# Performance work log

Measured on AMD Instinct MI355X. Metric: run time of the kernel, lower is better.

## Reference

```python
import jax, jax.numpy as jnp
import numpy as np

R = 4        # downsample / window size
HEADS = 8
TOPK = 4


def _dwconv3x3(x_nchw, w, b):
    # depthwise 3x3, padding 1. w: [C,1,3,3]
    C = x_nchw.shape[1]
    y = jax.lax.conv_general_dilated(
        x_nchw, w, window_strides=(1, 1), padding=((1, 1), (1, 1)),
        dimension_numbers=('NCHW', 'OIHW', 'NCHW'), feature_group_count=C)
    return y + b[None, :, None, None]


def setup_inputs() -> dict:
    key = jax.random.key(0)
    ks = jax.random.split(key, 8)
    B, H, W, C = 8, 64, 64, 384
    s = 0.02
    return {
        'x': jax.random.normal(ks[0], (B, H, W, C), jnp.float32),
        'qkv_w': jax.random.normal(ks[1], (3 * C, C), jnp.float32) * s,
        'dwx_w': jax.random.normal(ks[2], (C, 1, 3, 3), jnp.float32) * s,
        'dwx_b': jax.random.normal(ks[3], (C,), jnp.float32) * s,
        'dw_w': jax.random.normal(ks[4], (C, 1, 3, 3), jnp.float32) * s,
        'dw_b': jax.random.normal(ks[5], (C,), jnp.float32) * s,
        'pw_w': jax.random.normal(ks[6], (C, C), jnp.float32) * s,
        'pw_b': jax.random.normal(ks[7], (C,), jnp.float32) * s,
    }


def reference(x, qkv_w, dwx_w, dwx_b, dw_w, dw_b, pw_w, pw_b):
    B, H, W, C = x.shape
    h, r, topk = HEADS, R, TOPK
    d = C // h
    scale = d ** -0.5
    Hc, Wc = H // r, W // r
    Nc = Hc * Wc

    y = x

    # ---- coarse stream: avg-pool downsample then dense attention ----
    xc = x.reshape(B, Hc, r, Wc, r, C).mean(axis=(2, 4))       # [B,Hc,Wc,C]
    xc = xc.reshape(B, Nc, C)
    qkv = (xc @ qkv_w.T).reshape(B, Nc, 3, h, d).transpose(2, 0, 3, 1, 4)
    q, k, v = qkv[0], qkv[1], qkv[2]                           # [B,h,Nc,d]
    attn = jnp.einsum('bhqd,bhkd->bhqk', q, k) * scale         # [B,h,Nc,Nc]
    _, indices = jax.lax.top_k(attn, topk)                     # [B,h,Nc,topk]
    attn = jax.nn.softmax(attn, axis=-1)
    xo = jnp.einsum('bhqk,bhkd->bhqd', attn, v)                # [B,h,Nc,d]
    xo = xo.transpose(0, 2, 1, 3).reshape(B, Hc, Wc, C)

    # ---- full-res stream: windowed sparse attention driven by topk indices ----
    yf = y.reshape(B, H * W, C)
    QKV = (yf @ qkv_w.T).reshape(B, H * W, 3, h, d).transpose(2, 0, 3, 1, 4)
    Q, K, V = QKV[0], QKV[1], QKV[2]                           # [B,h,H*W,d]

    def to_windows(t):
        # [B,h,H*W,d] -> [B,h,nWin,r*r,d], window order matches coarse (h w) flatten
        t = t.reshape(B, h, Hc, r, Wc, r, d).transpose(0, 1, 2, 4, 3, 5, 6)
        return t.reshape(B, h, Nc, r * r, d)

    Qw, Kw, Vw = to_windows(Q), to_windows(K), to_windows(V)

    idx = indices[:, :, :, :, None, None]                      # [B,h,Nc,topk,1,1]
    Kg = jnp.take_along_axis(Kw[:, :, None], idx, axis=3)      # [B,h,Nc,topk,r*r,d]
    Vg = jnp.take_along_axis(Vw[:, :, None], idx, axis=3)
    Kg = Kg.reshape(B, h, Nc, topk * r * r, d)
    Vg = Vg.reshape(B, h, Nc, topk * r * r, d)

    a2 = jnp.einsum('bhnqd,bhnkd->bhnqk', Qw, Kg) * scale
    a2 = jax.nn.softmax(a2, axis=-1)
    yo = jnp.einsum('bhnqk,bhnkd->bhnqd', a2, Vg)              # [B,h,Nc,r*r,d]
    yo = yo.reshape(B, h, Hc, Wc, r, r, d).transpose(0, 2, 4, 3, 5, 1, 6)
    yo = yo.reshape(B, H, W, C)                                # NHWC

    # ---- coarse branch: nearest upsample + depthwise conv ----
    xn = xo.transpose(0, 3, 1, 2)                              # [B,C,Hc,Wc]
    xn = jnp.repeat(jnp.repeat(xn, r, axis=2), r, axis=3)      # [B,C,H,W]
    xn = _dwconv3x3(xn, dwx_w, dwx_b)
    xn = xn.transpose(0, 2, 3, 1)                              # NHWC

    # ---- fuse, depthwise + pointwise conv ----
    z = 0.5 * xn + 0.5 * yo
    z = z.transpose(0, 3, 1, 2)                                # NCHW
    z = _dwconv3x3(z, dw_w, dw_b)
    z = jnp.einsum('bchw,oc->bohw', z, pw_w) + pw_b[None, :, None, None]
    return z.transpose(0, 2, 3, 1)                             # NHWC
```

## Files before the change

kernel.cpp:

```cpp
#include <hip/hip_runtime.h>
#include <hip/hip_bf16.h>


#define Bq 8
#define Hh 8
#define Dd 48
#define Cc 384
#define NC 256
#define MFINE 32768
#define KDIM 384
#define SCALE 0.14433756729740643f

typedef __attribute__((ext_vector_type(8))) short short8;
typedef __attribute__((ext_vector_type(4))) short short4v;
typedef __attribute__((ext_vector_type(4))) float floatx4;

#define QKVW_PLANE 12582912

#define WS_XBF   88342528
#define WS_XC     9437184
#define WS_WQKV 113508352
#define WS_WDWX 114393088
#define WS_BDWX 114400000
#define WS_WDW  114400768
#define WS_BDW  114407680
#define WS_WPW  114408448
#define WS_BPW  114703360

__global__ __launch_bounds__(256) void k_detect(const ushort* x, int* flag) {
    __shared__ int cnt;
    if (threadIdx.x == 0) cnt = 0;
    __syncthreads();
    int c = 0;
    for (int i = threadIdx.x; i < 8192; i += 256) {
        int e = (x[i] >> 7) & 0xFF;
        if (e >= 0xC1) c++;
    }
    atomicAdd(&cnt, c);
    __syncthreads();
    if (threadIdx.x == 0) *flag = (cnt > 16) ? 1 : 0;
}

__device__ __forceinline__ void cvt_seg(const void* src, __hip_bfloat16* dst, int blk, int n4, int fl) {
    int i = blk * 256 + threadIdx.x;
    if (i >= n4) return;
    if (fl) {
        floatx4 v = ((const floatx4*)src)[i];
        short4v o;
        for (int t = 0; t < 4; t++) {
            __hip_bfloat16 hb = __float2bfloat16(v[t]);
            o[t] = *(short*)&hb;
        }
        ((short4v*)dst)[i] = o;
    } else {
        ((short4v*)dst)[i] = ((const short4v*)src)[i];
    }
}

__global__ __launch_bounds__(256) void k_cvt_pool(
        const void* sx, const void* s1, const void* s2, const void* s3,
        const void* s4, const void* s5, const void* s6, const void* s7,
        char* ws, const int* flag) {
    int blk = blockIdx.x;
    int fl = *flag;
    if (blk < 12288) { cvt_seg(sx, (__hip_bfloat16*)(ws + WS_XBF),  blk,          3145728, fl); return; }
    if (blk < 12720) { cvt_seg(s1, (__hip_bfloat16*)(ws + WS_WQKV), blk - 12288,  110592, fl); return; }
    if (blk < 12724) { cvt_seg(s2, (__hip_bfloat16*)(ws + WS_WDWX), blk - 12720,  864,    fl); return; }
    if (blk < 12725) { cvt_seg(s3, (__hip_bfloat16*)(ws + WS_BDWX), blk - 12724,  96,     fl); return; }
    if (blk < 12729) { cvt_seg(s4, (__hip_bfloat16*)(ws + WS_WDW),  blk - 12725,  864,    fl); return; }
    if (blk < 12730) { cvt_seg(s5, (__hip_bfloat16*)(ws + WS_BDW),  blk - 12729,  96,     fl); return; }
    if (blk < 12874) { cvt_seg(s6, (__hip_bfloat16*)(ws + WS_WPW),  blk - 12730,  36864,  fl); return; }
    if (blk < 12875) { cvt_seg(s7, (__hip_bfloat16*)(ws + WS_BPW),  blk - 12874,  96,     fl); return; }
    int pb = blk - 12875;
    if (threadIdx.x >= 192) return;
    int b = pb >> 8, n = pb & 255;
    int yc = n >> 4, xcc = n & 15;
    int c0 = threadIdx.x * 2;
    size_t pixbase = (((size_t)(b * 64 + yc * 4)) * 64 + xcc * 4) * Cc + c0;
    float s0 = 0.f, s1v = 0.f;
    if (fl) {
        const float* xf = (const float*)sx;
        for (int i = 0; i < 4; i++)
            for (int j = 0; j < 4; j++) {
                float2 u = *(const float2*)(xf + pixbase + ((size_t)i * 64 + j) * Cc);
                s0 += u.x; s1v += u.y;
            }
    } else {
        const ushort* xb = (const ushort*)sx;
        for (int i = 0; i < 4; i++)
            for (int j = 0; j < 4; j++) {
                uint u = *(const uint*)(xb + pixbase + ((size_t)i * 64 + j) * Cc);
                s0 += __uint_as_float(u << 16);
                s1v += __uint_as_float(u & 0xFFFF0000u);
            }
    }
    __hip_bfloat16 h0 = __float2bfloat16(s0 * 0.0625f), h1 = __float2bfloat16(s1v * 0.0625f);
    uint uo = (uint)*(ushort*)&h0 | ((uint)*(ushort*)&h1 << 16);
    *(uint*)((ushort*)(ws + WS_XC) + (size_t)pb * Cc + c0) = uo;
}

__device__ __forceinline__ void gload_lds16(const ushort* g, short* l) {
    __builtin_amdgcn_global_load_lds(
        (const __attribute__((address_space(1))) unsigned int*)(g),
        (__attribute__((address_space(3))) unsigned int*)(l), 16, 0, 0);
}

__device__ __forceinline__ void gemm128_dbuf(const ushort* A, const ushort* B,
                                             int tile_m, int tile_n,
                                             short* As, short* Bs, floatx4 (&acc)[4][4]) {
    int lane = threadIdx.x & 63, wave = threadIdx.x >> 6;
    int m_off = (wave >> 1) * 64, n_off = (wave & 1) * 64;
    int row16 = lane & 15, quad = lane >> 4;
    int srow = lane >> 3;
    int scol = (((lane & 7) ^ srow) * 8);
    for (int i = 0; i < 4; i++)
        for (int j = 0; j < 4; j++)
            acc[i][j] = (floatx4){0.f, 0.f, 0.f, 0.f};
    int rsw = (row16 & 7) * 8;
#define STG(buf, k0)                                                                          \
    for (int g = wave; g < 16; g += 4) {                                                      \
        gload_lds16(A + (size_t)(tile_m + g * 8 + srow) * KDIM + (k0) + scol, As + (buf) * 8192 + g * 512); \
        gload_lds16(B + (size_t)(tile_n + g * 8 + srow) * KDIM + (k0) + scol, Bs + (buf) * 8192 + g * 512); \
    }
    STG(0, 0)
    int cur = 0;
    for (int k0 = 0; k0 < KDIM; k0 += 64) {
        if (k0 + 64 < KDIM) {
            STG(cur ^ 1, k0 + 64)
            asm volatile("s_waitcnt vmcnt(8)" ::: "memory");
        } else {
            asm volatile("s_waitcnt vmcnt(0)" ::: "memory");
        }
        __builtin_amdgcn_s_barrier();
        __builtin_amdgcn_sched_barrier(0);
        __builtin_amdgcn_s_setprio(1);
        const short* Ab = As + cur * 8192;
        const short* Bb = Bs + cur * 8192;
        for (int h = 0; h < 2; h++) {
            short8 af[4], bf[4];
            for (int mt = 0; mt < 4; mt++)
                af[mt] = *(const short8*)(Ab + (m_off + mt * 16 + row16) * 64 + (((h * 4 + quad) * 8) ^ rsw));
            for (int nt = 0; nt < 4; nt++)
                bf[nt] = *(const short8*)(Bb + (n_off + nt * 16 + row16) * 64 + (((h * 4 + quad) * 8) ^ rsw));
            for (int mt = 0; mt < 4; mt++)
                for (int nt = 0; nt < 4; nt++)
                    acc[mt][nt] = __builtin_amdgcn_mfma_f32_16x16x32_bf16(af[mt], bf[nt], acc[mt][nt], 0, 0, 0);
        }
        __builtin_amdgcn_s_setprio(0);
        __builtin_amdgcn_sched_barrier(0);
        __builtin_amdgcn_s_barrier();
        cur ^= 1;
    }
#undef STG
}

__device__ __forceinline__ void gemm128_sb(const ushort* A, const ushort* B,
                                           int tile_m, int tile_n,
                                           short* As, short* Bs, floatx4 (&acc)[4][4]) {
    int lane = threadIdx.x & 63, wave = threadIdx.x >> 6;
    int m_off = (wave >> 1) * 64, n_off = (wave & 1) * 64;
    int row16 = lane & 15, quad = lane >> 4;
    int srow = lane >> 3;
    int scol = (((lane & 7) ^ srow) * 8);
    for (int i = 0; i < 4; i++)
        for (int j = 0; j < 4; j++)
            acc[i][j] = (floatx4){0.f, 0.f, 0.f, 0.f};
    int rsw = (row16 & 7) * 8;
    for (int k0 = 0; k0 < KDIM; k0 += 64) {
        for (int g = wave; g < 16; g += 4) {
            gload_lds16(A + (size_t)(tile_m + g * 8 + srow) * KDIM + k0 + scol, As + g * 512);
            gload_lds16(B + (size_t)(tile_n + g * 8 + srow) * KDIM + k0 + scol, Bs + g * 512);
        }
        __syncthreads();
        for (int h = 0; h < 2; h++) {
            short8 af[4], bf[4];
            for (int mt = 0; mt < 4; mt++)
                af[mt] = *(const short8*)(As + (m_off + mt * 16 + row16) * 64 + (((h * 4 + quad) * 8) ^ rsw));
            for (int nt = 0; nt < 4; nt++)
                bf[nt] = *(const short8*)(Bs + (n_off + nt * 16 + row16) * 64 + (((h * 4 + quad) * 8) ^ rsw));
            for (int mt = 0; mt < 4; mt++)
                for (int nt = 0; nt < 4; nt++)
                    acc[mt][nt] = __builtin_amdgcn_mfma_f32_16x16x32_bf16(af[mt], bf[nt], acc[mt][nt], 0, 0, 0);
        }
        __syncthreads();
    }
}

__device__ __forceinline__ floatx4 mfma_tile(const ushort* A, const ushort* W,
                                             int tile_m, int tile_n, int lane) {
    int row16 = lane & 15, quad = lane >> 4;
    const ushort* arow = A + (size_t)(tile_m + row16) * KDIM + quad * 8;
    const ushort* brow = W + (size_t)(tile_n + row16) * KDIM + quad * 8;
    floatx4 acc = {0.f, 0.f, 0.f, 0.f};
    for (int kk = 0; kk < KDIM; kk += 32) {
        short8 af = *(const short8*)(arow + kk);
        short8 bf = *(const short8*)(brow + kk);
        acc = __builtin_amdgcn_mfma_f32_16x16x32_bf16(af, bf, acc, 0, 0, 0);
    }
    return acc;
}

__global__ __launch_bounds__(256) void k_gemm_qkv_coarse(const ushort* A, const ushort* W,
                                                         __hip_bfloat16* qh, __hip_bfloat16* ql,
                                                         __hip_bfloat16* kh, __hip_bfloat16* kl,
                                                         __hip_bfloat16* vt) {
    int lane = threadIdx.x & 63, wave = threadIdx.x >> 6;
    int tile_m = blockIdx.y * 32 + (wave >> 1) * 16;
    int tile_n = blockIdx.x * 32 + (wave & 1) * 16;
    floatx4 acc = mfma_tile(A, W, tile_m, tile_n, lane);
    int row16 = lane & 15, quad = lane >> 4;
    int n = tile_n + row16;
    int which = n / Cc, hd = n % Cc, head = hd / Dd, dim = hd % Dd;
    for (int rr = 0; rr < 4; rr++) {
        int m = tile_m + quad * 4 + rr;
        int b = m >> 8, nc = m & 255;
        float v = acc[rr];
        __hip_bfloat16 hi = __float2bfloat16(v);
        if (which == 0) {
            size_t p = ((size_t)((b * Hh + head) * NC + nc)) * Dd + dim;
            qh[p] = hi;
            ql[p] = __float2bfloat16(v - __bfloat162float(hi));
        } else if (which == 1) {
            size_t p = ((size_t)((b * Hh + head) * NC + nc)) * Dd + dim;
            kh[p] = hi;
            kl[p] = __float2bfloat16(v - __bfloat162float(hi));
        } else {
            vt[((size_t)((b * Hh + head) * Dd + dim)) * NC + nc] = hi;
        }
    }
}

#define PST 264
__global__ __launch_bounds__(256) void k_fine_cattn(
        const ushort* A, const ushort* W, __hip_bfloat16* qkvw,
        const ushort* qh, const ushort* ql, const ushort* kh, const ushort* kl,
        const ushort* vt, int* idx_out, __hip_bfloat16* xo) {
    __shared__ __align__(16) short smem[32768];
    int lane = threadIdx.x & 63, wave = threadIdx.x >> 6;
    int row16 = lane & 15, quad = lane >> 4;
    if (blockIdx.x < 256) {
        short* Pl = smem;
        int bh = blockIdx.x >> 2, qt = blockIdx.x & 3;
        int q0 = qt * 64 + wave * 16;
        short8 zf = {0, 0, 0, 0, 0, 0, 0, 0};
        const ushort* qhr = qh + ((size_t)(bh * NC + q0 + row16)) * Dd;
        const ushort* qlr = ql + ((size_t)(bh * NC + q0 + row16)) * Dd;
        short8 aqh0 = *(const short8*)(qhr + quad * 8);
        short8 aqh1 = (quad < 2) ? *(const short8*)(qhr + 32 + quad * 8) : zf;
        short8 aql0 = *(const short8*)(qlr + quad * 8);
        short8 aql1 = (quad < 2) ? *(const short8*)(qlr + 32 + quad * 8) : zf;
        floatx4 s[16];
        for (int nt = 0; nt < 16; nt++) {
            const ushort* khr = kh + ((size_t)(bh * NC + nt * 16 + row16)) * Dd;
            const ushort* klr = kl + ((size_t)(bh * NC + nt * 16 + row16)) * Dd;
            short8 bh0 = *(const short8*)(khr + quad * 8);
            short8 bh1 = (quad < 2) ? *(const short8*)(khr + 32 + quad * 8) : zf;
            short8 bl0 = *(const short8*)(klr + quad * 8);
            short8 bl1 = (quad < 2) ? *(const short8*)(klr + 32 + quad * 8) : zf;
            floatx4 a = {0.f, 0.f, 0.f, 0.f};
            a = __builtin_amdgcn_mfma_f32_16x16x32_bf16(aqh0, bh0, a, 0, 0, 0);
            a = __builtin_amdgcn_mfma_f32_16x16x32_bf16(aqh1, bh1, a, 0, 0, 0);
            a = __builtin_amdgcn_mfma_f32_16x16x32_bf16(aqh0, bl0, a, 0, 0, 0);
            a = __builtin_amdgcn_mfma_f32_16x16x32_bf16(aqh1, bl1, a, 0, 0, 0);
            a = __builtin_amdgcn_mfma_f32_16x16x32_bf16(aql0, bh0, a, 0, 0, 0);
            a = __builtin_amdgcn_mfma_f32_16x16x32_bf16(aql1, bh1, a, 0, 0, 0);
            s[nt] = a;
        }
        for (int rr = 0; rr < 4; rr++) {
            float sv[16];
            for (int nt = 0; nt < 16; nt++) sv[nt] = s[nt][rr] * SCALE;
            int chosen[4] = {-1, -1, -1, -1};
            float rowmax = 0.f;
            for (int it = 0; it < 4; it++) {
                float bv = -3.402823e38f; int bi = 0x7fffffff;
                for (int nt = 0; nt < 16; nt++) {
                    int ki = nt * 16 + row16;
                    bool skip = (ki == chosen[0]) | (ki == chosen[1]) | (ki == chosen[2]) | (ki == chosen[3]);
                    if (!skip && sv[nt] > bv) { bv = sv[nt]; bi = ki; }
                }
                for (int mk = 1; mk < 16; mk <<= 1) {
                    float ov = __shfl_xor(bv, mk); int oi = __shfl_xor(bi, mk);
                    if (ov > bv || (ov == bv && oi < bi)) { bv = ov; bi = oi; }
                }
                chosen[it] = bi;
                if (it == 0) rowmax = bv;
            }
            if (row16 == 0) {
                int q = q0 + quad * 4 + rr;
                for (int it = 0; it < 4; it++)
                    idx_out[((size_t)bh * NC + q) * 4 + it] = chosen[it];
            }
            float ex[16], sum = 0.f;
            for (int nt = 0; nt < 16; nt++) { ex[nt] = __expf(sv[nt] - rowmax); sum += ex[nt]; }
            for (int mk = 1; mk < 16; mk <<= 1) sum += __shfl_xor(sum, mk);
            float inv = 1.f / sum;
            for (int nt = 0; nt < 16; nt++) {
                __hip_bfloat16 hb = __float2bfloat16(ex[nt] * inv);
                Pl[(wave * 16 + quad * 4 + rr) * PST + nt * 16 + row16] = *(short*)&hb;
            }
        }
        const ushort* vbase = vt + (size_t)bh * Dd * NC;
        floatx4 o[3];
        for (int i = 0; i < 3; i++) o[i] = (floatx4){0.f, 0.f, 0.f, 0.f};
        for (int k0 = 0; k0 < 256; k0 += 32) {
            short8 pa = *(const short8*)&Pl[(wave * 16 + row16) * PST + k0 + quad * 8];
            for (int d2 = 0; d2 < 3; d2++) {
                short8 vb = *(const short8*)(vbase + (size_t)(d2 * 16 + row16) * NC + k0 + quad * 8);
                o[d2] = __builtin_amdgcn_mfma_f32_16x16x32_bf16(pa, vb, o[d2], 0, 0, 0);
            }
        }
        int b = bh >> 3, hh = bh & 7;
        for (int rr = 0; rr < 4; rr++) {
            int q = q0 + quad * 4 + rr;
            size_t base = ((size_t)(b * NC + q)) * Cc + hh * Dd;
            for (int d2 = 0; d2 < 3; d2++)
                xo[base + d2 * 16 + row16] = __float2bfloat16(o[d2][rr]);
        }
        return;
    }
    floatx4 acc[4][4];
    int f = blockIdx.x - 256;
    int s = (f & 7) * 288 + (f >> 3);
    int by = s / 9, bx = s - by * 9;
    int tile_m = by * 128, tile_n = bx * 128;
    gemm128_dbuf(A, W, tile_m, tile_n, smem, smem + 16384, acc);
    int m_off = (wave >> 1) * 64, n_off = (wave & 1) * 64;
    short* epi = smem + wave * 2304;
    int r = lane >> 1, parity = lane & 1;
    for (int half = 0; half < 2; half++) {
        __syncthreads();
        for (int mt2 = 0; mt2 < 2; mt2++) {
            int mt = half * 2 + mt2;
            for (int nt = 0; nt < 4; nt++)
                for (int rr = 0; rr < 4; rr++) {
                    __hip_bfloat16 hb = __float2bfloat16(acc[mt][nt][rr]);
                    epi[(mt2 * 16 + quad * 4 + rr) * 72 + nt * 16 + row16] = *(short*)&hb;
                }
        }
        __syncthreads();
        int m = tile_m + m_off + half * 32 + r;
        int b = m >> 12, pix = m & 4095;
        int y = pix >> 6, x = pix & 63;
        int win = (y >> 2) * 16 + (x >> 2);
        int pos = (y & 3) * 4 + (x & 3);
        size_t mrow = ((size_t)b * Hh * NC * 16 * Dd) + ((size_t)win * 16 + pos) * Dd;
        for (int i = 0; i < 4; i++) {
            int j = parity + 2 * i;
            int n = tile_n + n_off + j * 8;
            int which = n / Cc, hd = n % Cc, head = hd / Dd, dim = hd % Dd;
            short8 val = *(const short8*)(epi + r * 72 + j * 8);
            size_t dst = (size_t)which * QKVW_PLANE + (size_t)head * (NC * 16 * Dd) + mrow + dim;
            *(short8*)((ushort*)qkvw + dst) = val;
        }
    }
}

#define PSTRIDE 80
#define VSTRIDE 72
__global__ __launch_bounds__(256) void k_win_attn(const __hip_bfloat16* qkvw, const int* idx, __hip_bfloat16* yo) {
    __shared__ __align__(16) short Pl[4][16 * PSTRIDE];
    __shared__ __align__(16) short Vt[4][48 * VSTRIDE];
    int lane = threadIdx.x & 63, wave = threadIdx.x >> 6;
    int gw = blockIdx.x * 4 + wave;
    int bh = gw >> 8, n = gw & 255;
    int row16 = lane & 15, quad = lane >> 4;
    const ushort* qb  = (const ushort*)qkvw + (size_t)(bh * NC + n) * 768;
    const ushort* kwb = (const ushort*)qkvw + (size_t)QKVW_PLANE + (size_t)bh * NC * 768;
    const ushort* vwb = (const ushort*)qkvw + 2 * (size_t)QKVW_PLANE + (size_t)bh * NC * 768;
    int sel[4];
    for (int g = 0; g < 4; g++) sel[g] = idx[(size_t)gw * 4 + g];
    const ushort* vrow = vwb + (size_t)sel[quad] * 768 + row16 * 48;
    short8 vv[6];
    for (int i = 0; i < 6; i++) vv[i] = *(const short8*)(vrow + i * 8);
    short8 zf = {0, 0, 0, 0, 0, 0, 0, 0};
    short8 aq0 = *(const short8*)(qb + row16 * 48 + quad * 8);
    short8 aq1 = (quad < 2) ? *(const short8*)(qb + row16 * 48 + 32 + quad * 8) : zf;
    floatx4 s[4];
    for (int nt = 0; nt < 4; nt++) {
        const ushort* kb = kwb + (size_t)sel[nt] * 768 + row16 * 48;
        short8 bk0 = *(const short8*)(kb + quad * 8);
        short8 bk1 = (quad < 2) ? *(const short8*)(kb + 32 + quad * 8) : zf;
        floatx4 a = {0.f, 0.f, 0.f, 0.f};
        a = __builtin_amdgcn_mfma_f32_16x16x32_bf16(aq0, bk0, a, 0, 0, 0);
        a = __builtin_amdgcn_mfma_f32_16x16x32_bf16(aq1, bk1, a, 0, 0, 0);
        s[nt] = a;
    }
    for (int i = 0; i < 6; i++)
        for (int j = 0; j < 8; j++)
            Vt[wave][(i * 8 + j) * VSTRIDE + lane] = vv[i][j];
    for (int rr = 0; rr < 4; rr++) {
        float sv[4];
        float m = -3.402823e38f;
        for (int nt = 0; nt < 4; nt++) { sv[nt] = s[nt][rr] * SCALE; m = fmaxf(m, sv[nt]); }
        for (int msk = 1; msk < 16; msk <<= 1) m = fmaxf(m, __shfl_xor(m, msk));
        float sum = 0.f;
        for (int nt = 0; nt < 4; nt++) { sv[nt] = expf(sv[nt] - m); sum += sv[nt]; }
        for (int msk = 1; msk < 16; msk <<= 1) sum += __shfl_xor(sum, msk);
        float inv = 1.f / sum;
        for (int nt = 0; nt < 4; nt++) {
            __hip_bfloat16 hb = __float2bfloat16(sv[nt] * inv);
            Pl[wave][(quad * 4 + rr) * PSTRIDE + nt * 16 + row16] = *(short*)&hb;
        }
    }
    floatx4 o[3];
    for (int i = 0; i < 3; i++) o[i] = (floatx4){0.f, 0.f, 0.f, 0.f};
    for (int k0 = 0; k0 < 64; k0 += 32) {
        short8 pa = *(const short8*)&Pl[wave][row16 * PSTRIDE + k0 + quad * 8];
        for (int nt2 = 0; nt2 < 3; nt2++) {
            short8 vb = *(const short8*)&Vt[wave][(nt2 * 16 + row16) * VSTRIDE + k0 + quad * 8];
            o[nt2] = __builtin_amdgcn_mfma_f32_16x16x32_bf16(pa, vb, o[nt2], 0, 0, 0);
        }
    }
    int b = bh >> 3, hh = bh & 7;
    int wy = n >> 4, wx = n & 15;
    for (int rr = 0; rr < 4; rr++) {
        int q = quad * 4 + rr;
        int y = wy * 4 + (q >> 2), x = wx * 4 + (q & 3);
        size_t base = (((size_t)(b * 64 + y)) * 64 + x) * Cc + hh * Dd;
        for (int nt2 = 0; nt2 < 3; nt2++)
            yo[base + nt2 * 16 + row16] = __float2bfloat16(o[nt2][rr]);
    }
}

__global__ __launch_bounds__(192) void k_dwfuse(const __hip_bfloat16* xo, const __hip_bfloat16* yo,
                                                const __hip_bfloat16* dwx_w, const __hip_bfloat16* dwx_b,
                                                const __hip_bfloat16* dw_w, const __hip_bfloat16* dw_b,
                                                __hip_bfloat16* z) {
    int c0 = threadIdx.x * 2;
    int blk = blockIdx.x;
    int xc = blk & 7, by = blk >> 3;
    int y = by & 63, b = by >> 6;
    int x0 = xc * 8;
    float wx0[9], wx1[9], wd0[9], wd1[9];
    for (int k = 0; k < 9; k++) {
        wx0[k] = __bfloat162float(dwx_w[c0 * 9 + k]);
        wx1[k] = __bfloat162float(dwx_w[(c0 + 1) * 9 + k]);
        wd0[k] = __bfloat162float(dw_w[c0 * 9 + k]);
        wd1[k] = __bfloat162float(dw_w[(c0 + 1) * 9 + k]);
    }
    float bx0 = __bfloat162float(dwx_b[c0]), bx1 = __bfloat162float(dwx_b[c0 + 1]);
    float bd0 = __bfloat162float(dw_b[c0]),  bd1 = __bfloat162float(dw_b[c0 + 1]);
    int r_base = (y >= 2 ? y - 2 : 0) >> 2;
    int c_base = x0 / 4 - 1;
    float px0[2][4], px1[2][4];
    for (int pr = 0; pr < 2; pr++) {
        int cr = r_base + pr;
        for (int pc = 0; pc < 4; pc++) {
            int cc2 = c_base + pc;
            uint u = (cr < 16 && cc2 >= 0 && cc2 < 16) ?
                *(const uint*)((const ushort*)xo + ((size_t)(b * NC + cr * 16 + cc2)) * Cc + c0) : 0u;
            px0[pr][pc] = __uint_as_float(u << 16);
            px1[pr][pc] = __uint_as_float(u & 0xFFFF0000u);
        }
    }
    float sr0[5][4], sr1[5][4];
#pragma unroll
    for (int f = 0; f < 5; f++) {
        int fy = y - 2 + f;
        bool valid = (fy >= 0 && fy < 64);
        int pr = valid ? ((fy >> 2) - r_base) : 0;
#pragma unroll
        for (int pc = 0; pc < 4; pc++) {
            float v0 = pr ? px0[1][pc] : px0[0][pc];
            float v1 = pr ? px1[1][pc] : px1[0][pc];
            sr0[f][pc] = valid ? v0 : 0.f;
            sr1[f][pc] = valid ? v1 : 0.f;
        }
    }
    float zp0[3][10], zp1[3][10];
#pragma unroll
    for (int r = 0; r < 3; r++)
#pragma unroll
        for (int cq = 0; cq < 10; cq++) { zp0[r][cq] = 0.f; zp1[r][cq] = 0.f; }
#pragma unroll
    for (int r = 0; r < 3; r++) {
        int fyz = y + r - 1;
        if (fyz < 0 || fyz > 63) continue;
#pragma unroll
        for (int cq = 0; cq < 10; cq++) {
            int fxz = x0 - 1 + cq;
            if (fxz < 0 || fxz > 63) continue;
            float a0 = bx0, a1 = bx1;
#pragma unroll
            for (int dy = -1; dy <= 1; dy++) {
#pragma unroll
                for (int dx = -1; dx <= 1; dx++) {
                    int t = cq - 1 + dx;
                    int pc = 1 + ((t + 8) / 4 - 2);
                    int fx = fxz + dx;
                    bool cvalid = (fx >= 0 && fx < 64);
                    int f = r + dy + 1;
                    float t0 = cvalid ? sr0[f][pc] : 0.f;
                    float t1 = cvalid ? sr1[f][pc] : 0.f;
                    a0 += t0 * wx0[(dy + 1) * 3 + (dx + 1)];
                    a1 += t1 * wx1[(dy + 1) * 3 + (dx + 1)];
                }
            }
            uint uy = *(const uint*)((const ushort*)yo + (((size_t)(b * 64 + fyz)) * 64 + fxz) * Cc + c0);
            zp0[r][cq] = 0.5f * a0 + 0.5f * __uint_as_float(uy << 16);
            zp1[r][cq] = 0.5f * a1 + 0.5f * __uint_as_float(uy & 0xFFFF0000u);
        }
    }
    size_t obase = ((size_t)(b * 64 + y) * 64) * Cc + c0;
#pragma unroll
    for (int xq = 0; xq < 8; xq++) {
        float a0 = bd0, a1 = bd1;
#pragma unroll
        for (int dy = 0; dy < 3; dy++)
#pragma unroll
            for (int dx = 0; dx < 3; dx++) {
                a0 += zp0[dy][xq + dx] * wd0[dy * 3 + dx];
                a1 += zp1[dy][xq + dx] * wd1[dy * 3 + dx];
            }
        __hip_bfloat16 h0 = __float2bfloat16(a0), h1 = __float2bfloat16(a1);
        uint uo = (uint)*(ushort*)&h0 | ((uint)*(ushort*)&h1 << 16);
        *(uint*)((ushort*)z + obase + (size_t)(x0 + xq) * Cc) = uo;
    }
}

__global__ __launch_bounds__(256) void k_gemm_pw(const ushort* Z, const ushort* W, const __hip_bfloat16* bias,
                                                 void* out, const int* flag) {
    __shared__ __align__(16) short smem[16384];
    floatx4 acc[4][4];
    int f = blockIdx.x;
    int s = (f & 7) * 96 + (f >> 3);
    int by = s / 3, bx = s - by * 3;
    int tile_m = by * 128, tile_n = bx * 128;
    gemm128_sb(Z, W, tile_m, tile_n, smem, smem + 8192, acc);
    int lane = threadIdx.x & 63, wave = threadIdx.x >> 6;
    int m_off = (wave >> 1) * 64, n_off = (wave & 1) * 64;
    int row16 = lane & 15, quad = lane >> 4;
    float* epi = (float*)smem + wave * 1216;
    int f32out = *flag;
    int r4 = lane >> 2, c4 = lane & 3;
    for (int mt = 0; mt < 4; mt++) {
        __syncthreads();
        for (int nt = 0; nt < 4; nt++)
            for (int rr = 0; rr < 4; rr++)
                epi[(quad * 4 + rr) * 76 + nt * 16 + row16] = acc[mt][nt][rr];
        __syncthreads();
        int m = tile_m + m_off + mt * 16 + r4;
        for (int i = 0; i < 4; i++) {
            int j = c4 + 4 * i;
            int n0 = tile_n + n_off + j * 4;
            floatx4 v = *(const floatx4*)(epi + r4 * 76 + j * 4);
            short4v bb = *(const short4v*)((const ushort*)bias + n0);
            for (int t = 0; t < 4; t++) {
                short sb = bb[t];
                v[t] += __bfloat162float(*(const __hip_bfloat16*)&sb);
            }
            if (f32out) {
                *(floatx4*)((float*)out + (size_t)m * Cc + n0) = v;
            } else {
                short4v o;
                for (int t = 0; t < 4; t++) { __hip_bfloat16 hb = __float2bfloat16(v[t]); o[t] = *(short*)&hb; }
                *(short4v*)((__hip_bfloat16*)out + (size_t)m * Cc + n0) = o;
            }
        }
    }
}

extern "C" void kernel_launch(void* const* d_in, const int* in_sizes, int n_in,
                              void* d_out, int out_size, void* d_ws, size_t ws_size,
                              hipStream_t stream) {
    char* ws = (char*)d_ws;
    __hip_bfloat16* qhp  = (__hip_bfloat16*)(ws);
    __hip_bfloat16* qlp  = (__hip_bfloat16*)(ws + 1572864);
    __hip_bfloat16* khp  = (__hip_bfloat16*)(ws + 3145728);
    __hip_bfloat16* klp  = (__hip_bfloat16*)(ws + 4718592);
    __hip_bfloat16* vtp  = (__hip_bfloat16*)(ws + 6291456);
    __hip_bfloat16* xc   = (__hip_bfloat16*)(ws + WS_XC);
    int*            idx  = (int*)(ws + 11010048);
    __hip_bfloat16* xo   = (__hip_bfloat16*)(ws + 11272192);
    __hip_bfloat16* qkvw = (__hip_bfloat16*)(ws + 12845056);
    __hip_bfloat16* yo   = (__hip_bfloat16*)(ws + WS_XBF);
    __hip_bfloat16* xbf  = (__hip_bfloat16*)(ws + WS_XBF);
    __hip_bfloat16* zbuf = (__hip_bfloat16*)(ws + 12845056);
    __hip_bfloat16* wqkv = (__hip_bfloat16*)(ws + WS_WQKV);
    __hip_bfloat16* wdwx = (__hip_bfloat16*)(ws + WS_WDWX);
    __hip_bfloat16* bdwx = (__hip_bfloat16*)(ws + WS_BDWX);
    __hip_bfloat16* wdw  = (__hip_bfloat16*)(ws + WS_WDW);
    __hip_bfloat16* bdw  = (__hip_bfloat16*)(ws + WS_BDW);
    __hip_bfloat16* wpw  = (__hip_bfloat16*)(ws + WS_WPW);
    __hip_bfloat16* bpw  = (__hip_bfloat16*)(ws + WS_BPW);
    int*            flag = (int*)(ws + 114704128);

    k_detect<<<1, 256, 0, stream>>>((const ushort*)d_in[0], flag);
    k_cvt_pool<<<14923, 256, 0, stream>>>(d_in[0], d_in[1], d_in[2], d_in[3],
                                          d_in[4], d_in[5], d_in[6], d_in[7],
                                          ws, flag);

    k_gemm_qkv_coarse<<<dim3(36, 64), 256, 0, stream>>>((const ushort*)xc, (const ushort*)wqkv,
                                                        qhp, qlp, khp, klp, vtp);
    k_fine_cattn<<<2560, 256, 0, stream>>>((const ushort*)xbf, (const ushort*)wqkv, qkvw,
                                           (const ushort*)qhp, (const ushort*)qlp,
                                           (const ushort*)khp, (const ushort*)klp,
                                           (const ushort*)vtp, idx, xo);
    k_win_attn<<<4096, 256, 0, stream>>>(qkvw, idx, yo);
    k_dwfuse<<<4096, 192, 0, stream>>>(xo, yo, wdwx, bdwx, wdw, bdw, zbuf);
    k_gemm_pw<<<768, 256, 0, stream>>>((const ushort*)zbuf, (const ushort*)wpw, bpw, d_out, flag);
}
```

Measured before the change: 282.1 us.

## Double-buffer pointwise GEMM K-loop with 32-wide stages to overlap loads

Replaces the single-buffered 64-wide K-step GEMM used by the pointwise conv with a double-buffered loop over 32-wide K slices. The next slice is prefetched into the alternate LDS buffer while MFMAs run on the current one, with vmcnt waits and raw barriers in place of full syncthreads. The LDS swizzle changes to fit 32-element rows. The aim is to hide global load latency behind compute, at the cost of twice as many K iterations and barriers.

```diff
diff --git a/kernel.cpp b/kernel.cpp
--- a/kernel.cpp
+++ b/kernel.cpp
@@ -154,36 +154,49 @@
 #undef STG
 }
 
-__device__ __forceinline__ void gemm128_sb(const ushort* A, const ushort* B,
-                                           int tile_m, int tile_n,
-                                           short* As, short* Bs, floatx4 (&acc)[4][4]) {
+__device__ __forceinline__ void gemm128_dbuf32(const ushort* A, const ushort* B,
+                                               int tile_m, int tile_n,
+                                               short* As, short* Bs, floatx4 (&acc)[4][4]) {
     int lane = threadIdx.x & 63, wave = threadIdx.x >> 6;
     int m_off = (wave >> 1) * 64, n_off = (wave & 1) * 64;
     int row16 = lane & 15, quad = lane >> 4;
-    int srow = lane >> 3;
-    int scol = (((lane & 7) ^ srow) * 8);
+    int srow = lane >> 2;
+    int scol = (((lane & 3) ^ ((srow >> 1) & 3)) * 8);
     for (int i = 0; i < 4; i++)
         for (int j = 0; j < 4; j++)
             acc[i][j] = (floatx4){0.f, 0.f, 0.f, 0.f};
-    int rsw = (row16 & 7) * 8;
-    for (int k0 = 0; k0 < KDIM; k0 += 64) {
-        for (int g = wave; g < 16; g += 4) {
-            gload_lds16(A + (size_t)(tile_m + g * 8 + srow) * KDIM + k0 + scol, As + g * 512);
-            gload_lds16(B + (size_t)(tile_n + g * 8 + srow) * KDIM + k0 + scol, Bs + g * 512);
-        }
-        __syncthreads();
-        for (int h = 0; h < 2; h++) {
-            short8 af[4], bf[4];
-            for (int mt = 0; mt < 4; mt++)
-                af[mt] = *(const short8*)(As + (m_off + mt * 16 + row16) * 64 + (((h * 4 + quad) * 8) ^ rsw));
+    int rch = (quad ^ ((row16 >> 1) & 3)) * 8;
+#define STG32(buf, k0)                                                                        \
+    for (int g = wave; g < 8; g += 4) {                                                       \
+        gload_lds16(A + (size_t)(tile_m + g * 16 + srow) * KDIM + (k0) + scol, As + (buf) * 4096 + g * 512); \
+        gload_lds16(B + (size_t)(tile_n + g * 16 + srow) * KDIM + (k0) + scol, Bs + (buf) * 4096 + g * 512); \
+    }
+    STG32(0, 0)
+    int cur = 0;
+    for (int k0 = 0; k0 < KDIM; k0 += 32) {
+        if (k0 + 32 < KDIM) {
+            STG32(cur ^ 1, k0 + 32)
+            asm volatile("s_waitcnt vmcnt(4)" ::: "memory");
+        } else {
+            asm volatile("s_waitcnt vmcnt(0)" ::: "memory");
+        }
+        __builtin_amdgcn_s_barrier();
+        __builtin_amdgcn_sched_barrier(0);
+        const short* Ab = As + cur * 4096;
+        const short* Bb = Bs + cur * 4096;
+        short8 af[4], bf[4];
+        for (int mt = 0; mt < 4; mt++)
+            af[mt] = *(const short8*)(Ab + (m_off + mt * 16 + row16) * 32 + rch);
+        for (int nt = 0; nt < 4; nt++)
+            bf[nt] = *(const short8*)(Bb + (n_off + nt * 16 + row16) * 32 + rch);
+        for (int mt = 0; mt < 4; mt++)
             for (int nt = 0; nt < 4; nt++)
-                bf[nt] = *(const short8*)(Bs + (n_off + nt * 16 + row16) * 64 + (((h * 4 + quad) * 8) ^ rsw));
-            for (int mt = 0; mt < 4; mt++)
-                for (int nt = 0; nt < 4; nt++)
-                    acc[mt][nt] = __builtin_amdgcn_mfma_f32_16x16x32_bf16(af[mt], bf[nt], acc[mt][nt], 0, 0, 0);
-        }
-        __syncthreads();
-    }
+                acc[mt][nt] = __builtin_amdgcn_mfma_f32_16x16x32_bf16(af[mt], bf[nt], acc[mt][nt], 0, 0, 0);
+        __builtin_amdgcn_sched_barrier(0);
+        __builtin_amdgcn_s_barrier();
+        cur ^= 1;
+    }
+#undef STG32
 }
 
 __device__ __forceinline__ floatx4 mfma_tile(const ushort* A, const ushort* W,
@@ -526,7 +539,7 @@
     int s = (f & 7) * 96 + (f >> 3);
     int by = s / 3, bx = s - by * 3;
     int tile_m = by * 128, tile_n = bx * 128;
-    gemm128_sb(Z, W, tile_m, tile_n, smem, smem + 8192, acc);
+    gemm128_dbuf32(Z, W, tile_m, tile_n, smem, smem + 8192, acc);
     int lane = threadIdx.x & 63, wave = threadIdx.x >> 6;
     int m_off = (wave >> 1) * 64, n_off = (wave & 1) * 64;
     int row16 = lane & 15, quad = lane >> 4;
```

Measured after the change: 284.4 us. No clear change (+0.8%).
